# Kernel optimization log

Measured on AMD Instinct MI355X. Metric: run time of the kernel, lower is better.

The kernel has to match this reference:

```python
import jax, jax.numpy as jnp
import numpy as np

DIM = 3          # algebra dimension (3D Clifford algebra Cl(3,0))
NB = 2 ** DIM    # 8 blades
C_IN, C_OUT = 4, 4
K = 3            # conv kernel size
S = 48           # spatial size (== mask_size)
B = 4            # batch size
HID = 128


def _build_algebra():
    """Cayley table of Cl(3,0) with blades ordered by (grade, bitmask), and the
    path matrix M[p, bj, bk] = sum_bi cayley[bi,bj,bk] restricted to grade-triple p."""
    n = NB
    blades = sorted(range(n), key=lambda b: (bin(b).count('1'), b))
    idx = {b: i for i, b in enumerate(blades)}
    grades = np.array([bin(b).count('1') for b in blades])
    cay = np.zeros((n, n, n), dtype=np.float32)
    for a in range(n):
        for b in range(n):
            s = 1
            t = a >> 1
            while t:
                s *= (-1) ** bin(t & b).count('1')
                t >>= 1
            cay[idx[a], idx[b], idx[a ^ b]] = s  # Euclidean metric: no extra signs
    ng = DIM + 1
    path_id = -np.ones((ng, ng, ng), dtype=int)
    p = 0
    for gi in range(ng):
        for gj in range(ng):
            for gk in range(ng):
                if np.any(cay[np.ix_(np.where(grades == gi)[0], np.where(grades == gj)[0], np.where(grades == gk)[0])] != 0):
                    path_id[gi, gj, gk] = p
                    p += 1
    P = p  # == product_paths_sum == 20 for Cl(3,0)
    M = np.zeros((P, n, n), dtype=np.float32)
    for i in range(n):
        for j in range(n):
            for k in range(n):
                c = cay[i, j, k]
                if c != 0.0:
                    M[path_id[grades[i], grades[j], grades[k]], j, k] += c
    return M, P

CAYLEY_M, P = _build_algebra()


def _circular_mask(ks):
    c = (ks - 1) / 2.0
    zz, yy, xx = np.ogrid[:ks, :ks, :ks]
    d = np.sqrt((xx - c) ** 2 + (yy - c) ** 2 + (zz - c) ** 2)
    return (d <= c).astype(np.float32)


def _rel_pos_mv():
    """Kernel-grid offsets embedded as grade-1 multivectors: (K^3, NB)."""
    ax = np.linspace(-1.0, 1.0, K).astype(np.float32)
    gx, gy, gz = np.meshgrid(ax, ax, ax, indexing='ij')
    pos = np.stack([gx, gy, gz], -1).reshape(-1, DIM)
    mv = np.zeros((K ** DIM, NB), dtype=np.float32)
    mv[:, 1:1 + DIM] = pos  # grade-1 blade slots are indices 1..3
    return mv


def setup_inputs() -> dict:
    key = jax.random.key(0)
    ks = jax.random.split(key, 4)
    x = jax.random.normal(ks[0], (B, C_IN, S, S, S, NB), jnp.float32)
    w0 = jax.random.normal(ks[1], (2 * NB, HID), jnp.float32) / np.sqrt(2 * NB)
    w1 = jax.random.normal(ks[2], (HID, HID), jnp.float32) / np.sqrt(HID)
    w2 = jax.random.normal(ks[3], (HID, C_OUT * C_IN * P), jnp.float32) / np.sqrt(HID)
    return {
        'x': x,
        'w0': w0, 'b0': jnp.zeros((HID,), jnp.float32),
        'w1': w1, 'b1': jnp.zeros((HID,), jnp.float32),
        'w2': w2, 'b2': jnp.zeros((C_OUT * C_IN * P,), jnp.float32),
        'bias_param': jnp.zeros((C_OUT, 1, 1, 1, 1), jnp.float32),
    }


def reference(x, w0, b0, w1, b1, w2, b2, bias_param):
    # 1) masked global pooling -> per-sample per-blade condition (B, NB)
    mask = jnp.asarray(_circular_mask(S))
    cond = jnp.einsum('bcxyzn,xyz->bn', x, mask) / (mask.sum() * C_IN)

    # 2) per-sample dynamic kernel generation (vmapped kernel network)
    rel = jnp.asarray(_rel_pos_mv())               # (X, NB), X = K^3
    X = K ** DIM
    feat = jnp.concatenate([
        jnp.broadcast_to(rel[None], (B, X, NB)),
        jnp.broadcast_to(cond[:, None, :], (B, X, NB)),
    ], axis=-1)                                     # (B, X, 2*NB)
    h = jax.nn.gelu(feat @ w0 + b0)
    h = jax.nn.gelu(h @ w1 + b1)
    w = (h @ w2 + b2).reshape(B, X, C_OUT, C_IN, P)  # per-path geometric-product weights

    # 3) assemble blade-level kernel via sparse Cayley contraction
    M = jnp.asarray(CAYLEY_M)                       # (P, NB_in_blade, NB_out_blade)
    ker = jnp.einsum('bxoip,pjk->bokijx', w, M)     # (B, o, bk, i, bj, X)
    kernels = ker.reshape(B * C_OUT * NB, C_IN * NB, K, K, K)

    # 4) grouped conv: one kernel bank per sample (feature_group_count = B)
    inp = jnp.transpose(x, (0, 1, 5, 2, 3, 4)).reshape(1, B * C_IN * NB, S, S, S)
    out = jax.lax.conv_general_dilated(
        inp, kernels, window_strides=(1, 1, 1), padding='SAME',
        dimension_numbers=('NCDHW', 'OIDHW', 'NCDHW'), feature_group_count=B)
    out = out.reshape(B, C_OUT, NB, S, S, S)
    out = jnp.transpose(out, (0, 1, 3, 4, 5, 2))    # (B, c_out, S,S,S, NB)

    # 5) multivector bias embedded at blade dims (0,)
    bias = jnp.zeros((C_OUT, 1, 1, 1, NB), x.dtype).at[..., 0:1].set(bias_param)
    return out + bias
```

## Files before the change

### kernel.cpp

```cpp
#include <hip/hip_runtime.h>
#include <cmath>

#define SS 48
#define S3 110592
#define NB 8
#define CIN 4
#define COUT 4
#define HID 128
#define XT 27
#define NP 20
#define BATCH 4
#define PD 50
#define PD2 2500
#define PD3 125000
#define SLABV 648
#define SLABS 5184

typedef __attribute__((ext_vector_type(8))) short short8;
typedef __attribute__((ext_vector_type(4))) float f32x4;

struct Tables {
    int   pid[64];
    float sgn[64];
};

__device__ __forceinline__ unsigned short bf16_rne(float f) {
    union { float f; unsigned u; } c; c.f = f;
    unsigned r = c.u + 0x7FFF + ((c.u >> 16) & 1);
    return (unsigned short)(r >> 16);
}

__device__ __forceinline__ float gelu_tanh(float v) {
    const float c = 0.7978845608028654f;
    float u = c * (v + 0.044715f * v * v * v);
    return 0.5f * v * (1.0f + tanhf(u));
}

__global__ __launch_bounds__(256)
void pack_cond_kernel(const float* __restrict__ x, unsigned short* __restrict__ xb,
                      float* __restrict__ partial) {
    int b  = blockIdx.y;
    int pv = blockIdx.x * 256 + threadIdx.x;
    __shared__ float sacc[8];
    if (threadIdx.x < 8) sacc[threadIdx.x] = 0.0f;
    __syncthreads();
    float acc[8];
#pragma unroll
    for (int n = 0; n < 8; ++n) acc[n] = 0.0f;
    if (pv < PD3) {
        int zp = pv / PD2, rem = pv % PD2, yp = rem / PD, xp = rem % PD;
        int z = zp - 1, y = yp - 1, xx = xp - 1;
        unsigned short ob[32];
        bool interior = (unsigned)z < 48u && (unsigned)y < 48u && (unsigned)xx < 48u;
        if (interior) {
            int v = (z * 48 + y) * 48 + xx;
            float vals[32];
#pragma unroll
            for (int i = 0; i < 4; ++i) {
                const f32x4* p = (const f32x4*)(x + (((size_t)(b * 4 + i)) * S3 + v) * 8);
                f32x4 a = p[0], c4 = p[1];
                vals[i * 8 + 0] = a[0];  vals[i * 8 + 1] = a[1];
                vals[i * 8 + 2] = a[2];  vals[i * 8 + 3] = a[3];
                vals[i * 8 + 4] = c4[0]; vals[i * 8 + 5] = c4[1];
                vals[i * 8 + 6] = c4[2]; vals[i * 8 + 7] = c4[3];
            }
            int dx = 2 * xx - 47, dy = 2 * y - 47, dz = 2 * z - 47;
            if (dx * dx + dy * dy + dz * dz <= 2209) {
#pragma unroll
                for (int n = 0; n < 8; ++n)
                    acc[n] = vals[n] + vals[8 + n] + vals[16 + n] + vals[24 + n];
            }
#pragma unroll
            for (int k = 0; k < 32; ++k) ob[k] = bf16_rne(vals[k]);
        } else {
#pragma unroll
            for (int k = 0; k < 32; ++k) ob[k] = 0;
        }
        short8* dst = (short8*)(xb + ((size_t)b * PD3 + pv) * 32);
#pragma unroll
        for (int q = 0; q < 4; ++q) {
            short8 s;
#pragma unroll
            for (int e = 0; e < 8; ++e) s[e] = (short)ob[q * 8 + e];
            dst[q] = s;
        }
    }
#pragma unroll
    for (int n = 0; n < 8; ++n) {
        float a = acc[n];
        for (int off = 32; off; off >>= 1) a += __shfl_down(a, off);
        if ((threadIdx.x & 63) == 0) atomicAdd(&sacc[n], a);
    }
    __syncthreads();
    if (threadIdx.x < 8)
        partial[((size_t)b * 512 + blockIdx.x) * 8 + threadIdx.x] = sacc[threadIdx.x];
}

__global__ __launch_bounds__(320)
void mlp_fused(const float* __restrict__ partial,
               const float* __restrict__ w0, const float* __restrict__ b0,
               const float* __restrict__ w1, const float* __restrict__ b1,
               const float* __restrict__ w2, const float* __restrict__ b2,
               unsigned short* __restrict__ wb, float inv_norm, Tables tb) {
    int bx = blockIdx.x;
    int b = bx / XT, tap = bx % XT;
    int t = threadIdx.x;
    __shared__ float red[40][8];
    __shared__ float feat[16];
    __shared__ float h1[HID];
    __shared__ float h2[HID];
    __shared__ float wrow[320];
    {
        int ch = t & 7, seg = t >> 3;
        float s = 0.0f;
        for (int j = seg; j < 489; j += 40)
            s += partial[((size_t)b * 512 + j) * 8 + ch];
        red[seg][ch] = s;
    }
    __syncthreads();
    if (t < 8) {
        float s2 = 0.0f;
#pragma unroll
        for (int q = 0; q < 40; ++q) s2 += red[q][t];
        feat[8 + t] = s2 * inv_norm;
        float v = 0.0f;
        if (t == 1) v = (float)(tap / 9) - 1.0f;
        else if (t == 2) v = (float)((tap / 3) % 3) - 1.0f;
        else if (t == 3) v = (float)(tap % 3) - 1.0f;
        feat[t] = v;
    }
    __syncthreads();
    if (t < 128) {
        float s = b0[t];
#pragma unroll
        for (int k = 0; k < 16; ++k) s += feat[k] * w0[k * HID + t];
        h1[t] = gelu_tanh(s);
    }
    __syncthreads();
    if (t < 128) {
        float a0 = b1[t], a1 = 0.0f, a2 = 0.0f, a3 = 0.0f;
#pragma unroll
        for (int k = 0; k < HID; k += 4) {
            a0 += h1[k + 0] * w1[(k + 0) * HID + t];
            a1 += h1[k + 1] * w1[(k + 1) * HID + t];
            a2 += h1[k + 2] * w1[(k + 2) * HID + t];
            a3 += h1[k + 3] * w1[(k + 3) * HID + t];
        }
        h2[t] = gelu_tanh((a0 + a1) + (a2 + a3));
    }
    __syncthreads();
    {
        float a0 = b2[t], a1 = 0.0f, a2 = 0.0f, a3 = 0.0f;
#pragma unroll
        for (int k = 0; k < HID; k += 4) {
            a0 += h2[k + 0] * w2[(size_t)(k + 0) * 320 + t];
            a1 += h2[k + 1] * w2[(size_t)(k + 1) * 320 + t];
            a2 += h2[k + 2] * w2[(size_t)(k + 2) * 320 + t];
            a3 += h2[k + 3] * w2[(size_t)(k + 3) * 320 + t];
        }
        wrow[t] = (a0 + a1) + (a2 + a3);
    }
    __syncthreads();
    if (t < 128) {
        int m = t >> 2, cq = t & 3;
        int o = m >> 3, bk = m & 7;
        short8 sv;
#pragma unroll
        for (int e = 0; e < 8; ++e) {
            int c = cq * 8 + e;
            int i = c >> 3, bj = c & 7, jk = bj * 8 + bk;
            sv[e] = (short)bf16_rne(tb.sgn[jk] * wrow[o * 80 + i * 20 + tb.pid[jk]]);
        }
        int g  = (tap / 9) * 3 + (tap % 3);
        int ky = (tap % 9) / 3;
        int half = m >> 4, mm = m & 15;
        size_t tile = (size_t)(b * 27 + g * 3 + ky) * 1024;
        *(short8*)(wb + tile + half * 512 + (mm + cq * 16) * 8) = sv;
    }
}

__global__ __launch_bounds__(256, 3)
void conv_lds(const unsigned short* __restrict__ xb, const unsigned short* __restrict__ wb,
              const float* __restrict__ bias, float* __restrict__ out) {
    __shared__ __align__(16) short lds[4 * SLABS];
    int b  = blockIdx.y;
    int bx = blockIdx.x;
    int tx = bx % 3, ty = (bx / 3) % 12, tz = bx / 36;
    int X0 = tx * 16, Y0 = ty * 4, Z0 = tz * 4;
    int tid = threadIdx.x, lane = tid & 63, wave = tid >> 6;

    const unsigned short* xsrc = xb + (size_t)b * PD3 * 32 +
        ((size_t)Z0 * PD2 + (size_t)Y0 * PD + X0) * 32 + wave * 8;
#pragma unroll
    for (int k = 0; k < 11; ++k) {
        int h0 = k * 64, h = h0 + lane;
        if (h < SLABV) {
            int hz = h / 108, rem = h % 108, hy = rem / 18, hx = rem % 18;
            __builtin_amdgcn_global_load_lds(
                (const unsigned int*)(xsrc + ((size_t)hz * PD2 + hy * PD + hx) * 32),
                (unsigned int*)&lds[wave * SLABS + h0 * 8], 16, 0, 0);
        }
    }

    int col = lane & 15, kl = lane >> 4;
    const unsigned short* wgl = wb + (size_t)b * 27648 + lane * 8;
    __syncthreads();

    f32x4 acc[2][4];
#pragma unroll
    for (int mh = 0; mh < 2; ++mh)
#pragma unroll
        for (int r = 0; r < 4; ++r)
#pragma unroll
            for (int e = 0; e < 4; ++e) acc[mh][r][e] = 0.0f;

#pragma unroll
    for (int kz = 0; kz < 3; ++kz) {
        short8 wr[2][9];
#pragma unroll
        for (int mh = 0; mh < 2; ++mh)
#pragma unroll
            for (int t9 = 0; t9 < 9; ++t9)
                wr[mh][t9] = *(const short8*)(wgl + (size_t)(kz * 9 + t9) * 1024 + mh * 512);
#pragma unroll
        for (int kx = 0; kx < 3; ++kx) {
            const short* lb = &lds[kl * SLABS + ((wave + kz) * 108 + col + kx) * 8];
            short8 bfv[6];
#pragma unroll
            for (int u = 0; u < 6; ++u)
                bfv[u] = *(const short8*)(lb + u * 144);
#pragma unroll
            for (int ky = 0; ky < 3; ++ky) {
#pragma unroll
                for (int r = 0; r < 4; ++r) {
                    acc[0][r] = __builtin_amdgcn_mfma_f32_16x16x32_bf16(wr[0][kx * 3 + ky], bfv[r + ky], acc[0][r], 0, 0, 0);
                    acc[1][r] = __builtin_amdgcn_mfma_f32_16x16x32_bf16(wr[1][kx * 3 + ky], bfv[r + ky], acc[1][r], 0, 0, 0);
                }
            }
        }
    }

    int xc = X0 + col;
    int z  = Z0 + wave;
#pragma unroll
    for (int mh = 0; mh < 2; ++mh) {
        int m0 = kl * 4 + mh * 16;
        int o = m0 >> 3, bk0 = m0 & 7;
        float bi = (bk0 == 0) ? bias[o] : 0.0f;
#pragma unroll
        for (int r = 0; r < 4; ++r) {
            int y = Y0 + r;
            int vox = (z * 48 + y) * 48 + xc;
            f32x4 v = acc[mh][r];
            v[0] += bi;
            *(f32x4*)(out + (((size_t)(b * 4 + o)) * S3 + vox) * 8 + bk0) = v;
        }
    }
}

static inline int pc_host(int v) { return __builtin_popcount(v); }

extern "C" void kernel_launch(void* const* d_in, const int* in_sizes, int n_in,
                              void* d_out, int out_size, void* d_ws, size_t ws_size,
                              hipStream_t stream) {
    const float* x    = (const float*)d_in[0];
    const float* w0   = (const float*)d_in[1];
    const float* b0   = (const float*)d_in[2];
    const float* w1   = (const float*)d_in[3];
    const float* b1   = (const float*)d_in[4];
    const float* w2   = (const float*)d_in[5];
    const float* b2   = (const float*)d_in[6];
    const float* bias = (const float*)d_in[7];
    float* out = (float*)d_out;

    float* ws      = (float*)d_ws;
    float* partial = ws;
    unsigned short* wbb = (unsigned short*)(ws + 30272);
    unsigned short* xb  = wbb + 110592;

    int cnt = 0;
    for (int z = 0; z < SS; ++z) {
        int dz = 2 * z - 47;
        for (int y = 0; y < SS; ++y) {
            int dy = 2 * y - 47;
            for (int xx = 0; xx < SS; ++xx) {
                int dx = 2 * xx - 47;
                if (dx * dx + dy * dy + dz * dz <= 2209) ++cnt;
            }
        }
    }
    float inv_norm = 1.0f / ((float)cnt * (float)CIN);

    int pidtab[4][4][4];
    {
        bool ex[4][4][4] = {};
        for (int A = 0; A < 8; ++A)
            for (int B = 0; B < 8; ++B)
                ex[pc_host(A)][pc_host(B)][pc_host(A ^ B)] = true;
        int p = 0;
        for (int gi = 0; gi < 4; ++gi)
            for (int gj = 0; gj < 4; ++gj)
                for (int gk = 0; gk < 4; ++gk)
                    pidtab[gi][gj][gk] = ex[gi][gj][gk] ? p++ : -1;
    }
    static const int blades[8] = {0, 1, 2, 4, 3, 5, 6, 7};
    Tables tb;
    for (int bj = 0; bj < 8; ++bj) {
        for (int bk = 0; bk < 8; ++bk) {
            int bmj = blades[bj], bmk = blades[bk];
            int bma = bmj ^ bmk;
            int sgn = 1, t = bma >> 1;
            while (t) {
                if (pc_host(t & bmj) & 1) sgn = -sgn;
                t >>= 1;
            }
            tb.sgn[bj * 8 + bk] = (float)sgn;
            tb.pid[bj * 8 + bk] = pidtab[pc_host(bma)][pc_host(bmj)][pc_host(bmk)];
        }
    }

    pack_cond_kernel<<<dim3(489, BATCH), dim3(256), 0, stream>>>(x, xb, partial);
    mlp_fused<<<dim3(BATCH * XT), dim3(320), 0, stream>>>(partial, w0, b0, w1, b1, w2, b2,
                                                          wbb, inv_norm, tb);
    conv_lds<<<dim3(432, BATCH), dim3(256), 0, stream>>>(xb, wbb, bias, out);
}
```

Baseline: 72.14 us.

## Make conv kernel persistent with double-buffered LDS and register-resident weights

Replaces the one-tile-per-block conv launch with 256 persistent 512-thread blocks. Each block handles 6-7 tiles of one batch sample and double-buffers the input slab in LDS, so the next tile's global-to-LDS load overlaps the current tile's MFMAs. Each wave keeps all 27 weight fragments for its half of the output channels in registers, loaded once, which removes the per-kz weight reloads. The cost is higher register pressure (27 short8 per lane) and a barrier per tile. Some CUs may sit idle because there is only one wave of blocks.

```diff
diff --git a/kernel.cpp b/kernel.cpp
--- a/kernel.cpp
+++ b/kernel.cpp
@@ -179,82 +179,96 @@
     }
 }
 
-__global__ __launch_bounds__(256, 3)
+__global__ __launch_bounds__(512, 2)
 void conv_lds(const unsigned short* __restrict__ xb, const unsigned short* __restrict__ wb,
               const float* __restrict__ bias, float* __restrict__ out) {
-    __shared__ __align__(16) short lds[4 * SLABS];
-    int b  = blockIdx.y;
-    int bx = blockIdx.x;
-    int tx = bx % 3, ty = (bx / 3) % 12, tz = bx / 36;
-    int X0 = tx * 16, Y0 = ty * 4, Z0 = tz * 4;
+    __shared__ __align__(16) short lds[2][4 * SLABS];
+    int bid = blockIdx.x;
     int tid = threadIdx.x, lane = tid & 63, wave = tid >> 6;
-
-    const unsigned short* xsrc = xb + (size_t)b * PD3 * 32 +
-        ((size_t)Z0 * PD2 + (size_t)Y0 * PD + X0) * 32 + wave * 8;
-#pragma unroll
-    for (int k = 0; k < 11; ++k) {
-        int h0 = k * 64, h = h0 + lane;
-        if (h < SLABV) {
-            int hz = h / 108, rem = h % 108, hy = rem / 18, hx = rem % 18;
-            __builtin_amdgcn_global_load_lds(
-                (const unsigned int*)(xsrc + ((size_t)hz * PD2 + hy * PD + hx) * 32),
-                (unsigned int*)&lds[wave * SLABS + h0 * 8], 16, 0, 0);
-        }
-    }
-
+    int zs = wave >> 1, mh = wave & 1;
     int col = lane & 15, kl = lane >> 4;
-    const unsigned short* wgl = wb + (size_t)b * 27648 + lane * 8;
-    __syncthreads();
-
-    f32x4 acc[2][4];
-#pragma unroll
-    for (int mh = 0; mh < 2; ++mh)
+
+    int b = bid >> 6, k = bid & 63;
+    int start, cntt;
+    if (k < 48) { start = k * 7; cntt = 7; }
+    else        { start = 336 + (k - 48) * 6; cntt = 6; }
+
+    const unsigned short* xbb = xb + (size_t)b * PD3 * 32;
+
+    const unsigned short* wgl = wb + (size_t)b * 27648 + mh * 512 + lane * 8;
+    short8 wreg[27];
+#pragma unroll
+    for (int t27 = 0; t27 < 27; ++t27) {
+        const unsigned short* p = wgl + (size_t)t27 * 1024;
+        asm volatile("global_load_dwordx4 %0, %1, off" : "=v"(wreg[t27]) : "v"(p));
+    }
+
+    int sl = wave >> 1, hbase = (wave & 1) * 324;
+    auto stage = [&](int tau, int buf) {
+        int txx = tau % 3, tyy = (tau / 3) % 12, tzz = tau / 36;
+        const unsigned short* base = xbb +
+            ((size_t)(tzz * 4) * PD2 + (size_t)(tyy * 4) * PD + txx * 16) * 32 + sl * 8;
+#pragma unroll
+        for (int kk = 0; kk < 6; ++kk) {
+            int h0 = hbase + kk * 64;
+            int h  = h0 + lane;
+            if (h < hbase + 324) {
+                int hz = h / 108, rem = h % 108, hy = rem / 18, hx = rem % 18;
+                __builtin_amdgcn_global_load_lds(
+                    (const unsigned int*)(base + ((size_t)hz * PD2 + hy * PD + hx) * 32),
+                    (unsigned int*)&lds[buf][sl * SLABS + h0 * 8], 16, 0, 0);
+            }
+        }
+    };
+
+    stage(start, 0);
+    __syncthreads();
+
+    for (int i = 0; i < cntt; ++i) {
+        int tau = start + i;
+        if (i + 1 < cntt) stage(tau + 1, (i + 1) & 1);
+
+        int txx = tau % 3, tyy = (tau / 3) % 12, tzz = tau / 36;
+        const short* lbase = &lds[i & 1][kl * SLABS + (zs * 108 + col) * 8];
+
+        f32x4 acc[4];
 #pragma unroll
         for (int r = 0; r < 4; ++r)
 #pragma unroll
-            for (int e = 0; e < 4; ++e) acc[mh][r][e] = 0.0f;
-
-#pragma unroll
-    for (int kz = 0; kz < 3; ++kz) {
-        short8 wr[2][9];
-#pragma unroll
-        for (int mh = 0; mh < 2; ++mh)
-#pragma unroll
-            for (int t9 = 0; t9 < 9; ++t9)
-                wr[mh][t9] = *(const short8*)(wgl + (size_t)(kz * 9 + t9) * 1024 + mh * 512);
-#pragma unroll
-        for (int kx = 0; kx < 3; ++kx) {
-            const short* lb = &lds[kl * SLABS + ((wave + kz) * 108 + col + kx) * 8];
-            short8 bfv[6];
-#pragma unroll
-            for (int u = 0; u < 6; ++u)
-                bfv[u] = *(const short8*)(lb + u * 144);
-#pragma unroll
-            for (int ky = 0; ky < 3; ++ky) {
-#pragma unroll
-                for (int r = 0; r < 4; ++r) {
-                    acc[0][r] = __builtin_amdgcn_mfma_f32_16x16x32_bf16(wr[0][kx * 3 + ky], bfv[r + ky], acc[0][r], 0, 0, 0);
-                    acc[1][r] = __builtin_amdgcn_mfma_f32_16x16x32_bf16(wr[1][kx * 3 + ky], bfv[r + ky], acc[1][r], 0, 0, 0);
+            for (int e = 0; e < 4; ++e) acc[r][e] = 0.0f;
+
+#pragma unroll
+        for (int kz = 0; kz < 3; ++kz)
+#pragma unroll
+            for (int kx = 0; kx < 3; ++kx) {
+                const short* lb = lbase + (kz * 108 + kx) * 8;
+                short8 bfv[6];
+#pragma unroll
+                for (int u = 0; u < 6; ++u)
+                    bfv[u] = *(const short8*)(lb + u * 144);
+#pragma unroll
+                for (int ky = 0; ky < 3; ++ky) {
+                    short8 a = wreg[(kz * 3 + kx) * 3 + ky];
+#pragma unroll
+                    for (int r = 0; r < 4; ++r)
+                        acc[r] = __builtin_amdgcn_mfma_f32_16x16x32_bf16(a, bfv[r + ky], acc[r], 0, 0, 0);
                 }
             }
-        }
-    }
-
-    int xc = X0 + col;
-    int z  = Z0 + wave;
-#pragma unroll
-    for (int mh = 0; mh < 2; ++mh) {
+
+        int xc = txx * 16 + col;
+        int z  = tzz * 4 + zs;
         int m0 = kl * 4 + mh * 16;
         int o = m0 >> 3, bk0 = m0 & 7;
         float bi = (bk0 == 0) ? bias[o] : 0.0f;
 #pragma unroll
         for (int r = 0; r < 4; ++r) {
-            int y = Y0 + r;
+            int y = tyy * 4 + r;
             int vox = (z * 48 + y) * 48 + xc;
-            f32x4 v = acc[mh][r];
+            f32x4 v = acc[r];
             v[0] += bi;
             *(f32x4*)(out + (((size_t)(b * 4 + o)) * S3 + vox) * 8 + bk0) = v;
         }
+        __syncthreads();
     }
 }
 
@@ -322,5 +336,5 @@
     pack_cond_kernel<<<dim3(489, BATCH), dim3(256), 0, stream>>>(x, xb, partial);
     mlp_fused<<<dim3(BATCH * XT), dim3(320), 0, stream>>>(partial, w0, b0, w1, b1, w2, b2,
                                                           wbb, inv_norm, tb);
-    conv_lds<<<dim3(432, BATCH), dim3(256), 0, stream>>>(xb, wbb, bias, out);
-}
+    conv_lds<<<dim3(256), dim3(512), 0, stream>>>(xb, wbb, bias, out);
+}
```

Result: faster. 63.29 us (-12.3%).
